# Kernel tuning notes

Measured on AMD Instinct MI355X. Metric: run time of the kernel, lower is better.

Reference implementation:

```python
import jax, jax.numpy as jnp
import numpy as np

NUM_HEADS = 16
HEAD_DIM = 64
HIDDEN = NUM_HEADS * HEAD_DIM  # 1024
B, S = 2, 2048


def setup_inputs() -> dict:
    key = jax.random.key(0)
    ks = jax.random.split(key, 6)
    return {
        "hidden_states": jax.random.normal(ks[0], (B, S, HIDDEN), dtype=jnp.float32),
        "lora_state": jax.random.normal(ks[1], (B, S, 3 * HIDDEN), dtype=jnp.float32) * 0.02,
        "w_attn": jax.random.normal(ks[2], (HIDDEN, 3 * HIDDEN), dtype=jnp.float32) * 0.02,
        "b_attn": jax.random.normal(ks[3], (3 * HIDDEN,), dtype=jnp.float32) * 0.02,
        "w_proj": jax.random.normal(ks[4], (HIDDEN, HIDDEN), dtype=jnp.float32) * 0.02,
        "b_proj": jax.random.normal(ks[5], (HIDDEN,), dtype=jnp.float32) * 0.02,
    }


def reference(hidden_states, lora_state, w_attn, b_attn, w_proj, b_proj):
    b, s, d = hidden_states.shape
    # c_attn (GPT2 Conv1D: x @ W + b) plus LoRA correction added pre-split
    qkv = hidden_states @ w_attn + b_attn + lora_state  # [B,S,3D]
    q, k, v = jnp.split(qkv, 3, axis=-1)

    def split_heads(t):  # [B,S,D] -> [B,H,S,hd]
        return t.reshape(b, s, NUM_HEADS, HEAD_DIM).transpose(0, 2, 1, 3)

    q, k, v = split_heads(q), split_heads(k), split_heads(v)

    # eager attention: full [B,H,S,S] scores (faithful to the original)
    attn_weights = jnp.einsum("bhqd,bhkd->bhqk", q, k)
    attn_weights = attn_weights / jnp.asarray(HEAD_DIM ** 0.5, attn_weights.dtype)
    # causal mask via where with finfo.min, as in the torch code
    causal = jnp.tril(jnp.ones((s, s), dtype=bool))
    mask_value = jnp.finfo(attn_weights.dtype).min
    attn_weights = jnp.where(causal[None, None], attn_weights, mask_value)
    attn_weights = jax.nn.softmax(attn_weights, axis=-1)
    # dropout is identity in eval mode
    attn_output = jnp.einsum("bhqk,bhkd->bhqd", attn_weights, v)

    # merge heads [B,H,S,hd] -> [B,S,D]
    attn_output = attn_output.transpose(0, 2, 1, 3).reshape(b, s, d)
    attn_output = attn_output @ w_proj + b_proj
    return attn_output
```

## Files before the change

### kernel.cpp

```cpp
#include <hip/hip_runtime.h>
#include <hip/hip_bf16.h>
#include <cstdint>
#include <cstddef>

typedef unsigned short u16;
typedef unsigned int u32;
using f32x4  = __attribute__((ext_vector_type(4))) float;
using bf16x8 = __attribute__((ext_vector_type(8))) short;

__device__ __forceinline__ u16 f2bf(float f) {
    u32 u = __builtin_bit_cast(u32, f);
    u32 r = u + 0x7fffu + ((u >> 16) & 1u);
    return (u16)(r >> 16);
}
__device__ __forceinline__ float bf2f(u16 b) {
    u32 u = ((u32)b) << 16;
    return __builtin_bit_cast(float, u);
}

__device__ __forceinline__ void gload16(const u16* g, u16* l) {
    __builtin_amdgcn_global_load_lds(
        (const __attribute__((address_space(1))) void*)g,
        (__attribute__((address_space(3))) void*)l,
        16, 0, 0);
}

__global__ void k_convert(const float* __restrict__ src, u16* __restrict__ dst, int n4) {
    int i = blockIdx.x * blockDim.x + threadIdx.x;
    int stride = gridDim.x * blockDim.x;
    for (; i < n4; i += stride) {
        float4 v = ((const float4*)src)[i];
        ushort4 o;
        o.x = f2bf(v.x); o.y = f2bf(v.y); o.z = f2bf(v.z); o.w = f2bf(v.w);
        ((ushort4*)dst)[i] = o;
    }
}

__global__ void k_lorab(const float* __restrict__ lora, const float* __restrict__ b_attn,
                        u16* __restrict__ dst, int n4) {
    int i = blockIdx.x * blockDim.x + threadIdx.x;
    int stride = gridDim.x * blockDim.x;
    for (; i < n4; i += stride) {
        float4 v = ((const float4*)lora)[i];
        float4 bz = ((const float4*)b_attn)[i % 768];
        ushort4 o;
        o.x = f2bf(v.x + bz.x); o.y = f2bf(v.y + bz.y);
        o.z = f2bf(v.z + bz.z); o.w = f2bf(v.w + bz.w);
        ((ushort4*)dst)[i] = o;
    }
}

__global__ void k_tconv(const float* __restrict__ src, u16* __restrict__ dst, int K, int N) {
    __shared__ float tile[32][33];
    int nb = blockIdx.x * 32, kb = blockIdx.y * 32;
    int tx = threadIdx.x, ty = threadIdx.y;
    #pragma unroll
    for (int j = 0; j < 32; j += 8)
        tile[ty + j][tx] = src[(size_t)(kb + ty + j) * N + nb + tx];
    __syncthreads();
    #pragma unroll
    for (int j = 0; j < 32; j += 8)
        dst[(size_t)(nb + ty + j) * K + kb + tx] = f2bf(tile[tx][ty + j]);
}

__device__ __forceinline__ void gemm128_mainloop(const u16* __restrict__ A,
                                                 const u16* __restrict__ Bt,
                                                 int m0, int n0, f32x4 (&acc)[4][4]) {
    __shared__ __align__(16) u16 As[2][128][32];
    __shared__ __align__(16) u16 Bs[2][128][32];
    const int t = threadIdx.x;
    const int lane = t & 63, wave = t >> 6;
    const int wr = wave >> 1, wc = wave & 1;
    const int g = lane >> 4, lr = lane & 15;

    #pragma unroll
    for (int mi = 0; mi < 4; mi++)
        #pragma unroll
        for (int ni = 0; ni < 4; ni++)
            acc[mi][ni] = (f32x4){0.f, 0.f, 0.f, 0.f};

    const int q0 = wave * 128 + lane;
    const int q1 = q0 + 64;
    const int r0 = q0 >> 2, c0 = (q0 & 3) * 8;
    const int r1 = q1 >> 2, c1 = (q1 & 3) * 8;
    u16* lA0 = &As[0][0][0] + wave * 1024;
    u16* lA1 = &As[1][0][0] + wave * 1024;
    u16* lB0 = &Bs[0][0][0] + wave * 1024;
    u16* lB1 = &Bs[1][0][0] + wave * 1024;
    const u16* gA0 = A  + (size_t)(m0 + r0) * 1024 + c0;
    const u16* gA1 = A  + (size_t)(m0 + r1) * 1024 + c1;
    const u16* gB0 = Bt + (size_t)(n0 + r0) * 1024 + c0;
    const u16* gB1 = Bt + (size_t)(n0 + r1) * 1024 + c1;

    auto STAGE = [&](u16* la, u16* lb, int kt) {
        gload16(gA0 + kt, la);
        gload16(gA1 + kt, la + 512);
        gload16(gB0 + kt, lb);
        gload16(gB1 + kt, lb + 512);
    };
    auto COMPUTE = [&](const u16 (*Asb)[32], const u16 (*Bsb)[32]) {
        bf16x8 af[4], bfr[4];
        #pragma unroll
        for (int mi = 0; mi < 4; mi++)
            af[mi] = *(const bf16x8*)&Asb[wr * 64 + mi * 16 + lr][g * 8];
        #pragma unroll
        for (int ni = 0; ni < 4; ni++)
            bfr[ni] = *(const bf16x8*)&Bsb[wc * 64 + ni * 16 + lr][g * 8];
        #pragma unroll
        for (int mi = 0; mi < 4; mi++)
            #pragma unroll
            for (int ni = 0; ni < 4; ni++)
                acc[mi][ni] = __builtin_amdgcn_mfma_f32_16x16x32_bf16(af[mi], bfr[ni], acc[mi][ni], 0, 0, 0);
    };

    STAGE(lA0, lB0, 0);
    STAGE(lA1, lB1, 32);

    for (int kt = 0; kt < 1024; kt += 64) {
        asm volatile("s_waitcnt vmcnt(4)" ::: "memory");
        __builtin_amdgcn_s_barrier();
        COMPUTE(As[0], Bs[0]);
        __builtin_amdgcn_s_barrier();
        asm volatile("" ::: "memory");
        if (kt + 64 < 1024) {
            STAGE(lA0, lB0, kt + 64);
            asm volatile("s_waitcnt vmcnt(4)" ::: "memory");
        } else {
            asm volatile("s_waitcnt vmcnt(0)" ::: "memory");
        }
        __builtin_amdgcn_s_barrier();
        COMPUTE(As[1], Bs[1]);
        __builtin_amdgcn_s_barrier();
        asm volatile("" ::: "memory");
        if (kt + 96 < 1024)
            STAGE(lA1, lB1, kt + 96);
    }
}

__global__ __launch_bounds__(256) void k_gemm_qkv(const u16* __restrict__ Xb, const u16* __restrict__ Wab,
                                                  const u16* __restrict__ loraB,
                                                  u16* __restrict__ Qb, u16* __restrict__ Kb, u16* __restrict__ Vt) {
    const int bid = blockIdx.y * 24 + blockIdx.x;
    const int xcd = bid & 7, k = bid >> 3;
    const int xm = xcd & 3, xn = xcd >> 2;
    const int mt = xm * 8 + (k & 7);
    const int nt = xn * 12 + (k >> 3);
    const int m0 = mt * 128, n0 = nt * 128;

    f32x4 acc[4][4];
    gemm128_mainloop(Xb, Wab, m0, n0, acc);
    const int lane = threadIdx.x & 63, wave = threadIdx.x >> 6;
    const int wr = wave >> 1, wc = wave & 1, g = lane >> 4, lr = lane & 15;
    #pragma unroll
    for (int mi = 0; mi < 4; mi++)
        #pragma unroll
        for (int ni = 0; ni < 4; ni++)
            #pragma unroll
            for (int r = 0; r < 4; r++) {
                int m = m0 + wr * 64 + mi * 16 + g * 4 + r;
                int n = n0 + wc * 64 + ni * 16 + lr;
                float v = acc[mi][ni][r] + bf2f(loraB[(size_t)m * 3072 + n]);
                int which = n >> 10, rem = n & 1023, h = rem >> 6, hd = rem & 63;
                int b = m >> 11, s = m & 2047;
                size_t idx = ((size_t)(b * 16 + h) * 2048 + s) * 64 + hd;
                if (which == 0)      Qb[idx] = f2bf(v * 0.125f);
                else if (which == 1) Kb[idx] = f2bf(v);
                else Vt[((size_t)(b * 16 + h) * 64 + hd) * 2048 + s] = f2bf(v);
            }
}

__device__ __forceinline__ void attn_tile(const u16 (*Ks)[72], const u16 (*Vs)[72], u16 (*Ps)[72],
                                          int g, int lr, int rowq , int k0, bool diag,
                                          bf16x8 qf0, bf16x8 qf1,
                                          f32x4 (&accO)[4], float (&m_run)[4], float (&l_run)[4]) {
    f32x4 sc[4];
    #pragma unroll
    for (int ni = 0; ni < 4; ni++) {
        bf16x8 kf0 = *(const bf16x8*)&Ks[ni * 16 + lr][g * 8];
        bf16x8 kf1 = *(const bf16x8*)&Ks[ni * 16 + lr][32 + g * 8];
        f32x4 z = {0.f, 0.f, 0.f, 0.f};
        z = __builtin_amdgcn_mfma_f32_16x16x32_bf16(qf0, kf0, z, 0, 0, 0);
        z = __builtin_amdgcn_mfma_f32_16x16x32_bf16(qf1, kf1, z, 0, 0, 0);
        sc[ni] = z;
    }
    if (diag) {
        #pragma unroll
        for (int ni = 0; ni < 4; ni++)
            #pragma unroll
            for (int r = 0; r < 4; r++)
                if (k0 + ni * 16 + lr > rowq + g * 4 + r) sc[ni][r] = -INFINITY;
    }
    #pragma unroll
    for (int r = 0; r < 4; r++) {
        float mx = fmaxf(fmaxf(sc[0][r], sc[1][r]), fmaxf(sc[2][r], sc[3][r]));
        #pragma unroll
        for (int d = 1; d < 16; d <<= 1) mx = fmaxf(mx, __shfl_xor(mx, d, 64));
        float mnew = fmaxf(m_run[r], mx);
        float fsc = __expf(m_run[r] - mnew);
        float ls = 0.f;
        #pragma unroll
        for (int ni = 0; ni < 4; ni++) {
            float p = __expf(sc[ni][r] - mnew);
            sc[ni][r] = p;
            ls += p;
        }
        #pragma unroll
        for (int d = 1; d < 16; d <<= 1) ls += __shfl_xor(ls, d, 64);
        #pragma unroll
        for (int di = 0; di < 4; di++) accO[di][r] *= fsc;
        m_run[r] = mnew;
        l_run[r] = l_run[r] * fsc + ls;
    }
    #pragma unroll
    for (int ni = 0; ni < 4; ni++)
        #pragma unroll
        for (int r = 0; r < 4; r++)
            Ps[g * 4 + r][ni * 16 + lr] = f2bf(sc[ni][r]);
    #pragma unroll
    for (int e = 0; e < 2; e++) {
        bf16x8 pa = *(const bf16x8*)&Ps[lr][e * 32 + g * 8];
        #pragma unroll
        for (int di = 0; di < 4; di++) {
            bf16x8 vb = *(const bf16x8*)&Vs[di * 16 + lr][e * 32 + g * 8];
            accO[di] = __builtin_amdgcn_mfma_f32_16x16x32_bf16(pa, vb, accO[di], 0, 0, 0);
        }
    }
}

__global__ __launch_bounds__(256) void k_attn(const u16* __restrict__ Qb, const u16* __restrict__ Kb,
                                              const u16* __restrict__ Vt, u16* __restrict__ Ao) {
    __shared__ __align__(16) u16 Ks[64][72];
    __shared__ __align__(16) u16 Vs[64][72];
    __shared__ __align__(16) u16 Ps[4][16][72];
    const int i = blockIdx.x, bh = blockIdx.y;
    const int qtA = i, qtB = 31 - i;
    const int t = threadIdx.x, wave = t >> 6, lane = t & 63;
    const int g = lane >> 4, lr = lane & 15;
    const size_t bhO = (size_t)bh * (2048 * 64);
    const int q0A = qtA * 64, q0B = qtB * 64;
    const int rowqA = q0A + wave * 16, rowqB = q0B + wave * 16;

    bf16x8 qfA0 = *(const bf16x8*)(Qb + bhO + (size_t)(rowqA + lr) * 64 + g * 8);
    bf16x8 qfA1 = *(const bf16x8*)(Qb + bhO + (size_t)(rowqA + lr) * 64 + 32 + g * 8);
    bf16x8 qfB0 = *(const bf16x8*)(Qb + bhO + (size_t)(rowqB + lr) * 64 + g * 8);
    bf16x8 qfB1 = *(const bf16x8*)(Qb + bhO + (size_t)(rowqB + lr) * 64 + 32 + g * 8);

    f32x4 accA[4], accB[4];
    float mA[4], lA[4], mB[4], lB[4];
    #pragma unroll
    for (int x = 0; x < 4; x++) {
        accA[x] = (f32x4){0.f,0.f,0.f,0.f}; accB[x] = (f32x4){0.f,0.f,0.f,0.f};
        mA[x] = -INFINITY; lA[x] = 0.f; mB[x] = -INFINITY; lB[x] = 0.f;
    }

    const int sr0 = t >> 3,         sj0 = t & 7;
    const int sr1 = (t + 256) >> 3, sj1 = (t + 256) & 7;
    const u16* gK0 = Kb + bhO + (size_t)sr0 * 64 + sj0 * 8;
    const u16* gK1 = Kb + bhO + (size_t)sr1 * 64 + sj1 * 8;
    const u16* gV0 = Vt + bhO + (size_t)sr0 * 2048 + sj0 * 8;
    const u16* gV1 = Vt + bhO + (size_t)sr1 * 2048 + sj1 * 8;

    uint4 pk0 = *(const uint4*)(gK0);
    uint4 pk1 = *(const uint4*)(gK1);
    uint4 pv0 = *(const uint4*)(gV0);
    uint4 pv1 = *(const uint4*)(gV1);

    for (int kt = 0; kt <= qtB; ++kt) {
        const int k0 = kt * 64;
        __syncthreads();
        *(uint4*)&Ks[sr0][sj0 * 8] = pk0;
        *(uint4*)&Ks[sr1][sj1 * 8] = pk1;
        *(uint4*)&Vs[sr0][sj0 * 8] = pv0;
        *(uint4*)&Vs[sr1][sj1 * 8] = pv1;
        __syncthreads();

        if (kt < qtB) {
            const size_t kn = (size_t)(k0 + 64);
            pk0 = *(const uint4*)(gK0 + kn * 64);
            pk1 = *(const uint4*)(gK1 + kn * 64);
            pv0 = *(const uint4*)(gV0 + kn);
            pv1 = *(const uint4*)(gV1 + kn);
        }

        if (kt <= qtA)
            attn_tile(Ks, Vs, Ps[wave], g, lr, rowqA, k0, kt == qtA, qfA0, qfA1, accA, mA, lA);
        attn_tile(Ks, Vs, Ps[wave], g, lr, rowqB, k0, kt == qtB, qfB0, qfB1, accB, mB, lB);
    }

    const int b = bh >> 4, h = bh & 15;
    #pragma unroll
    for (int di = 0; di < 4; di++)
        #pragma unroll
        for (int r = 0; r < 4; r++) {
            int sA = rowqA + g * 4 + r;
            int sB = rowqB + g * 4 + r;
            Ao[((size_t)(b * 2048 + sA)) * 1024 + h * 64 + di * 16 + lr] = f2bf(accA[di][r] / lA[r]);
            Ao[((size_t)(b * 2048 + sB)) * 1024 + h * 64 + di * 16 + lr] = f2bf(accB[di][r] / lB[r]);
        }
}

__global__ __launch_bounds__(256) void k_gemm_proj(const u16* __restrict__ Ao, const u16* __restrict__ Wpb,
                                                   const float* __restrict__ b_proj, float* __restrict__ out) {
    const int bid = blockIdx.y * 8 + blockIdx.x;
    const int xcd = bid & 7, k = bid >> 3;
    const int xm = xcd & 3, xn = xcd >> 2;
    const int mt = xm * 8 + (k & 7);
    const int nt = xn * 4 + (k >> 3);
    const int m0 = mt * 128, n0 = nt * 128;

    f32x4 acc[4][4];
    gemm128_mainloop(Ao, Wpb, m0, n0, acc);
    const int lane = threadIdx.x & 63, wave = threadIdx.x >> 6;
    const int wr = wave >> 1, wc = wave & 1, g = lane >> 4, lr = lane & 15;
    #pragma unroll
    for (int mi = 0; mi < 4; mi++)
        #pragma unroll
        for (int ni = 0; ni < 4; ni++)
            #pragma unroll
            for (int r = 0; r < 4; r++) {
                int m = m0 + wr * 64 + mi * 16 + g * 4 + r;
                int n = n0 + wc * 64 + ni * 16 + lr;
                out[(size_t)m * 1024 + n] = acc[mi][ni][r] + b_proj[n];
            }
}

extern "C" void kernel_launch(void* const* d_in, const int* in_sizes, int n_in,
                              void* d_out, int out_size, void* d_ws, size_t ws_size,
                              hipStream_t stream) {
    const float* hidden = (const float*)d_in[0];
    const float* lora   = (const float*)d_in[1];
    const float* w_attn = (const float*)d_in[2];
    const float* b_attn = (const float*)d_in[3];
    const float* w_proj = (const float*)d_in[4];
    const float* b_proj = (const float*)d_in[5];
    float* out = (float*)d_out;

    char* ws = (char*)d_ws;
    u16* Xb   = (u16*)(ws + 0x0);
    u16* Wab  = (u16*)(ws + 0x800000);
    u16* Wpb  = (u16*)(ws + 0xE00000);
    u16* Qb   = (u16*)(ws + 0x1000000);
    u16* Kb   = (u16*)(ws + 0x1800000);
    u16* Vt   = (u16*)(ws + 0x2000000);
    u16* lorB = (u16*)(ws + 0x2800000);
    u16* Ao   = Xb;

    k_convert<<<1024, 256, 0, stream>>>(hidden, Xb, (2 * 2048 * 1024) / 4);
    k_lorab<<<2048, 256, 0, stream>>>(lora, b_attn, lorB, (4096 * 3072) / 4);
    k_tconv<<<dim3(96, 32), dim3(32, 8), 0, stream>>>(w_attn, Wab, 1024, 3072);
    k_tconv<<<dim3(32, 32), dim3(32, 8), 0, stream>>>(w_proj, Wpb, 1024, 1024);
    k_gemm_qkv<<<dim3(24, 32), 256, 0, stream>>>(Xb, Wab, lorB, Qb, Kb, Vt);
    k_attn<<<dim3(16, 32), 256, 0, stream>>>(Qb, Kb, Vt, Ao);
    k_gemm_proj<<<dim3(8, 32), 256, 0, stream>>>(Ao, Wpb, b_proj, out);
}
```

Before: 306.1 us.

## Write QKV GEMM output in place and scatter heads in a separate kernel

```diff
diff --git a/kernel.cpp b/kernel.cpp
--- a/kernel.cpp
+++ b/kernel.cpp
@@ -138,8 +138,7 @@
 }
 
 __global__ __launch_bounds__(256) void k_gemm_qkv(const u16* __restrict__ Xb, const u16* __restrict__ Wab,
-                                                  const u16* __restrict__ loraB,
-                                                  u16* __restrict__ Qb, u16* __restrict__ Kb, u16* __restrict__ Vt) {
+                                                  u16* __restrict__ C ) {
     const int bid = blockIdx.y * 24 + blockIdx.x;
     const int xcd = bid & 7, k = bid >> 3;
     const int xm = xcd & 3, xn = xcd >> 2;
@@ -151,6 +150,7 @@
     gemm128_mainloop(Xb, Wab, m0, n0, acc);
     const int lane = threadIdx.x & 63, wave = threadIdx.x >> 6;
     const int wr = wave >> 1, wc = wave & 1, g = lane >> 4, lr = lane & 15;
+    const float qs = (n0 < 1024) ? 0.125f : 1.0f;
     #pragma unroll
     for (int mi = 0; mi < 4; mi++)
         #pragma unroll
@@ -159,14 +159,36 @@
             for (int r = 0; r < 4; r++) {
                 int m = m0 + wr * 64 + mi * 16 + g * 4 + r;
                 int n = n0 + wc * 64 + ni * 16 + lr;
-                float v = acc[mi][ni][r] + bf2f(loraB[(size_t)m * 3072 + n]);
-                int which = n >> 10, rem = n & 1023, h = rem >> 6, hd = rem & 63;
-                int b = m >> 11, s = m & 2047;
-                size_t idx = ((size_t)(b * 16 + h) * 2048 + s) * 64 + hd;
-                if (which == 0)      Qb[idx] = f2bf(v * 0.125f);
-                else if (which == 1) Kb[idx] = f2bf(v);
-                else Vt[((size_t)(b * 16 + h) * 64 + hd) * 2048 + s] = f2bf(v);
+                size_t idx = (size_t)m * 3072 + n;
+                float v = acc[mi][ni][r] + bf2f(C[idx]);
+                C[idx] = f2bf(v * qs);
             }
+}
+
+__global__ __launch_bounds__(256) void k_scatter(const u16* __restrict__ C,
+                                                 u16* __restrict__ Qb, u16* __restrict__ Kb,
+                                                 u16* __restrict__ Vt) {
+    __shared__ u16 vt[32][72];
+    const int st = blockIdx.x, bh = blockIdx.y;
+    const int b = bh >> 4, h = bh & 15;
+    const int s0 = st * 32;
+    const int tid = threadIdx.x;
+    const int i = tid >> 3, j = tid & 7;
+    const size_t crow = (size_t)(b * 2048 + s0 + i) * 3072 + h * 64 + j * 8;
+    const size_t orow = ((size_t)bh * 2048 + s0 + i) * 64 + j * 8;
+
+    uint4 q = *(const uint4*)(C + crow);
+    *(uint4*)(Qb + orow) = q;
+    uint4 kk = *(const uint4*)(C + crow + 1024);
+    *(uint4*)(Kb + orow) = kk;
+    uint4 vv = *(const uint4*)(C + crow + 2048);
+    *(uint4*)(&vt[i][j * 8]) = vv;
+    __syncthreads();
+    const int hd = tid >> 2, jj = tid & 3;
+    u16 tmp[8];
+    #pragma unroll
+    for (int x = 0; x < 8; x++) tmp[x] = vt[jj * 8 + x][hd];
+    *(uint4*)(Vt + ((size_t)bh * 64 + hd) * 2048 + s0 + jj * 8) = *(uint4*)tmp;
 }
 
 __device__ __forceinline__ void attn_tile(const u16 (*Ks)[72], const u16 (*Vs)[72], u16 (*Ps)[72],
@@ -349,7 +371,8 @@
     k_lorab<<<2048, 256, 0, stream>>>(lora, b_attn, lorB, (4096 * 3072) / 4);
     k_tconv<<<dim3(96, 32), dim3(32, 8), 0, stream>>>(w_attn, Wab, 1024, 3072);
     k_tconv<<<dim3(32, 32), dim3(32, 8), 0, stream>>>(w_proj, Wpb, 1024, 1024);
-    k_gemm_qkv<<<dim3(24, 32), 256, 0, stream>>>(Xb, Wab, lorB, Qb, Kb, Vt);
+    k_gemm_qkv<<<dim3(24, 32), 256, 0, stream>>>(Xb, Wab, lorB);
+    k_scatter<<<dim3(64, 32), 256, 0, stream>>>(lorB, Qb, Kb, Vt);
     k_attn<<<dim3(16, 32), 256, 0, stream>>>(Qb, Kb, Vt, Ao);
     k_gemm_proj<<<dim3(8, 32), 256, 0, stream>>>(Ao, Wpb, b_proj, out);
 }
```

Result: faster. 278.5 us (-9.0%).
